# Kernel tuning notes

Measured on AMD Instinct MI355X. Metric: run time of the kernel, lower is better.

Reference implementation:

```python
import math
import jax, jax.numpy as jnp
import numpy as np

B, A, U, S, E, HYP, H = 16384, 32, 64, 2048, 32, 64, 4
ATTEND_REG_COEF = 1e-3


def setup_inputs() -> dict:
    key = jax.random.key(0)
    ks = jax.random.split(key, 12)
    sc = 0.05
    return {
        "agent_qs": jax.random.normal(ks[0], (B, A), jnp.float32),
        "states": jax.random.normal(ks[1], (B, S), jnp.float32),
        # per-head selector hypernet: Linear(S,HYP)+ReLU+Linear(HYP,E,no bias)
        "sel_w1": jax.random.normal(ks[2], (H, S, HYP), jnp.float32) * sc,
        "sel_b1": jax.random.normal(ks[3], (H, HYP), jnp.float32) * sc,
        "sel_w2": jax.random.normal(ks[4], (H, HYP, E), jnp.float32) * sc,
        # per-head key extractor: Linear(U,E,no bias)
        "key_w": jax.random.normal(ks[5], (H, U, E), jnp.float32) * sc,
        # V net: Linear(S,E)+ReLU+Linear(E,1)
        "v_w1": jax.random.normal(ks[6], (S, E), jnp.float32) * sc,
        "v_b1": jax.random.normal(ks[7], (E,), jnp.float32) * sc,
        "v_w2": jax.random.normal(ks[8], (E, 1), jnp.float32) * sc,
        "v_b2": jax.random.normal(ks[9], (1,), jnp.float32) * sc,
    }


def reference(agent_qs, states, sel_w1, sel_b1, sel_w2, key_w, v_w1, v_b1, v_w2, v_b2):
    # nonlinear=False, weighted_head=False, state_bias=True (defaults used here)
    unit_states = states[:, : A * U].reshape(-1, A, U)  # [B, A, U]

    # per-head selectors: [B, H, E]
    h1 = jax.nn.relu(jnp.einsum("bs,hsk->bhk", states, sel_w1) + sel_b1[None])
    selectors = jnp.einsum("bhk,hke->bhe", h1, sel_w2)

    # per-head, per-agent keys: [B, H, A, E]
    keys = jnp.einsum("bau,hue->bhae", unit_states, key_w)

    # attention logits [B, H, A] (matches selector @ stacked-keys in torch)
    logits = jnp.einsum("bhe,bhae->bha", selectors, keys)
    weights = jax.nn.softmax(logits / math.sqrt(E), axis=-1)  # [B, H, A]

    head_attend = jnp.sum(weights, axis=1)  # [B, A]

    v = jax.nn.relu(states @ v_w1 + v_b1) @ v_w2 + v_b2  # [B, 1]

    # coef * sum over heads of mean(logits_h ** 2)
    attend_mag_regs = ATTEND_REG_COEF * jnp.sum(jnp.mean(logits ** 2, axis=(0, 2)))

    # per-head entropy: -(p * log(p + 1e-8)).sum(agents).mean(batch) -> [H]
    head_entropies = -jnp.mean(
        jnp.sum(weights * jnp.log(weights + 1e-8), axis=-1), axis=0
    )

    return head_attend, v, attend_mag_regs, head_entropies
```

## Files before the change

kernel.cpp:

```cpp
#include <hip/hip_runtime.h>
#include <hip/hip_bf16.h>

#define B_N 16384
#define A_N 32
#define U_N 64
#define S_N 2048
#define E_N 32
#define HYP_N 64
#define H_N 4
#define NREAL 288
#define NPADG 320

#define H1B_STRIDE 264

#define WS_WT    0
#define WS_MB    1310720
#define WS_PMAG  (WS_MB + 32768)
#define WS_PENT  (WS_PMAG + 65536)
#define WS_T     (WS_PENT + 262144)
#define WS_HV    (WS_T + 16777216)

#define OUT_V   (B_N * A_N)
#define OUT_MAG (OUT_V + B_N)
#define OUT_ENT (OUT_MAG + 1)

typedef __attribute__((ext_vector_type(8))) short bf16x8_t;
typedef __attribute__((ext_vector_type(4))) float floatx4_t;

#define AS1(p) ((const __attribute__((address_space(1))) void*)(p))
#define AS3(p) ((__attribute__((address_space(3))) void*)(p))

__device__ __forceinline__ unsigned short f2b(float f) {
    union { float f; unsigned u; } v; v.f = f;
    unsigned r = v.u + 0x7FFFu + ((v.u >> 16) & 1u);
    return (unsigned short)(r >> 16);
}
__device__ __forceinline__ float b2f(unsigned x) {
    union { unsigned u; float f; } v; v.u = x << 16; return v.f;
}
__device__ __forceinline__ uint4 pack_bf16x8(float4 a0, float4 a1) {
    uint4 o;
    o.x = (unsigned)f2b(a0.x) | ((unsigned)f2b(a0.y) << 16);
    o.y = (unsigned)f2b(a0.z) | ((unsigned)f2b(a0.w) << 16);
    o.z = (unsigned)f2b(a1.x) | ((unsigned)f2b(a1.y) << 16);
    o.w = (unsigned)f2b(a1.z) | ((unsigned)f2b(a1.w) << 16);
    return o;
}

__global__ __launch_bounds__(256) void pack_w_kernel(
        const float* __restrict__ sel_w1, const float* __restrict__ v_w1,
        const float* __restrict__ sel_w2, const float* __restrict__ key_w,
        unsigned short* __restrict__ Wt, unsigned short* __restrict__ Mb) {
    int idx = blockIdx.x * 256 + threadIdx.x;
    if (idx < NPADG * S_N) {
        int n = idx >> 11;
        int k = idx & 2047;
        float val = 0.0f;
        if (n < 256) {
            int h = n >> 6, kk = n & 63;
            val = sel_w1[((size_t)h * S_N + k) * HYP_N + kk];
        } else if (n < NREAL) {
            val = v_w1[(size_t)k * E_N + (n - 256)];
        }
        Wt[idx] = f2b(val);
    } else if (idx < NPADG * S_N + H_N * U_N * HYP_N) {
        int j = idx - NPADG * S_N;
        int h = j >> 12, u = (j >> 6) & 63, k = j & 63;
        const float* kw = key_w + ((size_t)h * U_N + u) * E_N;
        const float* w2 = sel_w2 + ((size_t)h * HYP_N + k) * E_N;
        float s = 0.0f;
#pragma unroll
        for (int e = 0; e < E_N; ++e) s = fmaf(kw[e], w2[e], s);
        Mb[j] = f2b(s);
    }
}

#define FM_BM 64
#define FM_BK 64
#define NIT   (S_N / FM_BK)
#define ASM_SH (FM_BM * FM_BK)
#define BSM_SH (NPADG * FM_BK)

__global__ __launch_bounds__(512, 2) void gemm_t_kernel(
        const float* __restrict__ states, const unsigned short* __restrict__ Wt,
        const float* __restrict__ sel_b1, const float* __restrict__ v_b1,
        const unsigned short* __restrict__ Mb,
        float* __restrict__ tg, unsigned short* __restrict__ hv) {
    __shared__ __align__(16) char pool[2 * ASM_SH * 2 + 2 * BSM_SH * 2];
    unsigned short* Asm = (unsigned short*)pool;
    unsigned short* Bsm = (unsigned short*)(pool + 2 * ASM_SH * 2);
    unsigned short* h1b = (unsigned short*)pool;

    const int t = threadIdx.x;
    const int lane = t & 63;
    const int w = t >> 6;
    const int m0 = blockIdx.x * FM_BM;
    const int miw = (w & 1) * 32;
    const int nw = (w >> 1) * 80;

    const int ar = t >> 3, acl = t & 7;
    const float* ap = states + (size_t)(m0 + ar) * S_N + acl * 8;
    const int aph = acl ^ (ar & 7);

    floatx4_t acc[2][5] = {};
    float4 a0, a1;

    a0 = *(const float4*)(ap);
    a1 = *(const float4*)(ap + 4);
    *(uint4*)(Asm + (size_t)(ar * 8 + aph) * 8) = pack_bf16x8(a0, a1);
#pragma unroll
    for (int i = 0; i < 5; ++i) {
        int p = i * 512 + t, n = p >> 3, sl = p & 7;
        int cl = sl ^ (n & 7);
        __builtin_amdgcn_global_load_lds(AS1(Wt + (size_t)n * S_N + cl * 8),
                                         AS3(Bsm + p * 8), 16, 0, 0);
    }
    a0 = *(const float4*)(ap + FM_BK);
    a1 = *(const float4*)(ap + FM_BK + 4);
    __syncthreads();

    int cur = 0;
    for (int it = 0; it < NIT; ++it) {
        if (it < NIT - 1) {
            unsigned short* An = Asm + (cur ^ 1) * ASM_SH;
            unsigned short* Bn = Bsm + (cur ^ 1) * BSM_SH;
            int k0 = (it + 1) * FM_BK;
            *(uint4*)(An + (size_t)(ar * 8 + aph) * 8) = pack_bf16x8(a0, a1);
#pragma unroll
            for (int i = 0; i < 5; ++i) {
                int p = i * 512 + t, n = p >> 3, sl = p & 7;
                int cl = sl ^ (n & 7);
                __builtin_amdgcn_global_load_lds(
                    AS1(Wt + (size_t)n * S_N + k0 + cl * 8),
                    AS3(Bn + p * 8), 16, 0, 0);
            }
            if (it < NIT - 2) {
                const float* g = ap + (it + 2) * FM_BK;
                a0 = *(const float4*)(g);
                a1 = *(const float4*)(g + 4);
            }
        }
        const unsigned short* Ac = Asm + cur * ASM_SH;
        const unsigned short* Bc = Bsm + cur * BSM_SH;
#pragma unroll
        for (int s = 0; s < 2; ++s) {
            const int c = s * 4 + (lane >> 4);
            bf16x8_t afr[2];
#pragma unroll
            for (int mt = 0; mt < 2; ++mt) {
                int r = miw + mt * 16 + (lane & 15);
                afr[mt] = *(const bf16x8_t*)(Ac + r * 64 + (c ^ (r & 7)) * 8);
            }
#pragma unroll
            for (int nt = 0; nt < 5; ++nt) {
                int n = nw + nt * 16 + (lane & 15);
                bf16x8_t bfr = *(const bf16x8_t*)(Bc + n * 64 + (c ^ (n & 7)) * 8);
                acc[0][nt] = __builtin_amdgcn_mfma_f32_16x16x32_bf16(
                    afr[0], bfr, acc[0][nt], 0, 0, 0);
                acc[1][nt] = __builtin_amdgcn_mfma_f32_16x16x32_bf16(
                    afr[1], bfr, acc[1][nt], 0, 0, 0);
            }
        }
        __syncthreads();
        cur ^= 1;
    }

#pragma unroll
    for (int nt = 0; nt < 5; ++nt) {
        int n = nw + nt * 16 + (lane & 15);
        if (n < 256) {
            float bias = sel_b1[n];
#pragma unroll
            for (int mt = 0; mt < 2; ++mt)
#pragma unroll
                for (int rg = 0; rg < 4; ++rg) {
                    int r = miw + mt * 16 + (lane >> 4) * 4 + rg;
                    float v = acc[mt][nt][rg] + bias;
                    h1b[r * H1B_STRIDE + n] = f2b(v > 0.0f ? v : 0.0f);
                }
        } else if (n < NREAL) {
            int j = n - 256;
            float bias = v_b1[j];
#pragma unroll
            for (int mt = 0; mt < 2; ++mt)
#pragma unroll
                for (int rg = 0; rg < 4; ++rg) {
                    int r = miw + mt * 16 + (lane >> 4) * 4 + rg;
                    float v = acc[mt][nt][rg] + bias;
                    hv[(size_t)(m0 + r) * 32 + j] = f2b(v > 0.0f ? v : 0.0f);
                }
        }
    }
    __syncthreads();

    {
        const int h = w >> 1;
        const int rb = (w & 1) * 32;
        floatx4_t tacc[2][4] = {};
#pragma unroll
        for (int s = 0; s < 2; ++s) {
            int k0 = s * 32 + (lane >> 4) * 8;
            bf16x8_t afr[2];
#pragma unroll
            for (int mt = 0; mt < 2; ++mt)
                afr[mt] = *(const bf16x8_t*)(
                    h1b + (rb + mt * 16 + (lane & 15)) * H1B_STRIDE + h * 64 + k0);
#pragma unroll
            for (int ut = 0; ut < 4; ++ut) {
                int u = ut * 16 + (lane & 15);
                bf16x8_t bfr = *(const bf16x8_t*)(Mb + ((size_t)(h * U_N + u) * 64) + k0);
#pragma unroll
                for (int mt = 0; mt < 2; ++mt)
                    tacc[mt][ut] = __builtin_amdgcn_mfma_f32_16x16x32_bf16(
                        afr[mt], bfr, tacc[mt][ut], 0, 0, 0);
            }
        }
#pragma unroll
        for (int mt = 0; mt < 2; ++mt)
#pragma unroll
            for (int ut = 0; ut < 4; ++ut)
#pragma unroll
                for (int rg = 0; rg < 4; ++rg) {
                    int b = m0 + rb + mt * 16 + (lane >> 4) * 4 + rg;
                    int u = ut * 16 + (lane & 15);
                    tg[((size_t)b * H_N + h) * U_N + u] = tacc[mt][ut][rg];
                }
    }
}

#define L_BM 16

__global__ __launch_bounds__(256, 8) void attend_l_kernel(
        const float* __restrict__ states, const float* __restrict__ tg,
        const unsigned short* __restrict__ hv,
        const float* __restrict__ v_w2, const float* __restrict__ v_b2,
        float* __restrict__ out, float* __restrict__ pmag, float* __restrict__ pent) {
    const int t = threadIdx.x;
    const int lane = t & 63;
    const int w = t >> 6;
    const int m0 = blockIdx.x * L_BM;
    const int a = lane & 31, uh = lane >> 5;

    for (int rr = 0; rr < 4; ++rr) {
        const int b = m0 + w * 4 + rr;
        const float* up = states + (size_t)b * S_N + a * 64 + uh * 32;
        const float* tp = tg + (size_t)b * (H_N * U_N) + uh * 32;
        float pl[4] = {0.0f, 0.0f, 0.0f, 0.0f};
        float4 c0 = ((const float4*)up)[0];
        float4 c1 = ((const float4*)up)[1];
#pragma unroll
        for (int i = 0; i < 8; ++i) {
            float4 s4 = c0;
            c0 = c1;
            if (i < 6) c1 = ((const float4*)up)[i + 2];
#pragma unroll
            for (int h = 0; h < 4; ++h) {
                float4 t4 = *(const float4*)(tp + h * U_N + i * 4);
                pl[h] = fmaf(s4.x, t4.x, pl[h]);
                pl[h] = fmaf(s4.y, t4.y, pl[h]);
                pl[h] = fmaf(s4.z, t4.z, pl[h]);
                pl[h] = fmaf(s4.w, t4.w, pl[h]);
            }
        }
#pragma unroll
        for (int h = 0; h < 4; ++h)
            pl[h] += __shfl_xor(pl[h], 32, 64);

        float mg = pl[0]*pl[0] + pl[1]*pl[1] + pl[2]*pl[2] + pl[3]*pl[3];
#pragma unroll
        for (int o = 16; o > 0; o >>= 1) mg += __shfl_xor(mg, o, 32);

        float hatt = 0.0f;
        float entv[4];
#pragma unroll
        for (int h = 0; h < 4; ++h) {
            float x = pl[h] * 0.17677669529663687f;
            float p = __expf(x);
            float den = p, px = p * x;
#pragma unroll
            for (int o = 16; o > 0; o >>= 1) {
                den += __shfl_xor(den, o, 32);
                px  += __shfl_xor(px,  o, 32);
            }
            float inv = 1.0f / den;
            hatt = fmaf(p, inv, hatt);
            entv[h] = px * inv - __logf(den);
        }

        if (uh == 0) {
            out[(size_t)b * A_N + a] = hatt;
            float pv = b2f((unsigned)hv[(size_t)b * 32 + a]) * v_w2[a];
#pragma unroll
            for (int o = 16; o > 0; o >>= 1) pv += __shfl_xor(pv, o, 32);
            if (a == 0) {
                out[OUT_V + b] = pv + v_b2[0];
                pmag[b] = mg;
#pragma unroll
                for (int h = 0; h < 4; ++h) pent[(size_t)h * B_N + b] = entv[h];
            }
        }
    }
}

__global__ __launch_bounds__(256) void finalize_kernel(
        const float* __restrict__ pmag, const float* __restrict__ pent,
        float* __restrict__ out) {
    int which = blockIdx.x;
    const float* src = (which == 0) ? pmag : (pent + (size_t)(which - 1) * B_N);
    float s = 0.0f;
    for (int i = threadIdx.x; i < B_N; i += 256) s += src[i];
#pragma unroll
    for (int o = 32; o > 0; o >>= 1) s += __shfl_xor(s, o, 64);
    __shared__ float red[4];
    if ((threadIdx.x & 63) == 0) red[threadIdx.x >> 6] = s;
    __syncthreads();
    if (threadIdx.x == 0) {
        float tot = red[0] + red[1] + red[2] + red[3];
        if (which == 0) out[OUT_MAG] = 1e-3f * tot / (float)(B_N * A_N);
        else out[OUT_ENT + which - 1] = -tot / (float)B_N;
    }
}

extern "C" void kernel_launch(void* const* d_in, const int* in_sizes, int n_in,
                              void* d_out, int out_size, void* d_ws, size_t ws_size,
                              hipStream_t stream) {
    const float* states = (const float*)d_in[1];
    const float* sel_w1 = (const float*)d_in[2];
    const float* sel_b1 = (const float*)d_in[3];
    const float* sel_w2 = (const float*)d_in[4];
    const float* key_w  = (const float*)d_in[5];
    const float* v_w1   = (const float*)d_in[6];
    const float* v_b1   = (const float*)d_in[7];
    const float* v_w2   = (const float*)d_in[8];
    const float* v_b2   = (const float*)d_in[9];
    float* out = (float*)d_out;
    char* wsb  = (char*)d_ws;

    unsigned short* Wt  = (unsigned short*)(wsb + WS_WT);
    unsigned short* Mb  = (unsigned short*)(wsb + WS_MB);
    float* pmag         = (float*)(wsb + WS_PMAG);
    float* pent         = (float*)(wsb + WS_PENT);
    float* tg           = (float*)(wsb + WS_T);
    unsigned short* hv  = (unsigned short*)(wsb + WS_HV);

    pack_w_kernel<<<dim3((NPADG * S_N + H_N * U_N * HYP_N + 255) / 256),
                    dim3(256), 0, stream>>>(sel_w1, v_w1, sel_w2, key_w, Wt, Mb);
    gemm_t_kernel<<<dim3(B_N / FM_BM), dim3(512), 0, stream>>>(
        states, Wt, sel_b1, v_b1, Mb, tg, hv);
    attend_l_kernel<<<dim3(B_N / L_BM), dim3(256), 0, stream>>>(
        states, tg, hv, v_w2, v_b2, out, pmag, pent);
    finalize_kernel<<<dim3(5), dim3(256), 0, stream>>>(pmag, pent, out);
}
```

Baseline: 301.5 us.

## Halve GEMM row tile and drop LDS double buffering for higher occupancy

The fused states×weights GEMM kernel now uses 32-row tiles with 256 threads (4 waves, each covering 80 output columns) instead of 64 rows with 512 threads. The A and B shared-memory tiles lose their double buffering, which cuts LDS per block to about 45 KB so several blocks can be resident per CU and the grid doubles. The cost is that each block reloads the full 320-column weight tile for half as many rows, doubling weight traffic. Single buffering also adds a second barrier per K step, so loads no longer overlap with the MFMA work inside a block.

```diff
diff --git a/kernel.cpp b/kernel.cpp
--- a/kernel.cpp
+++ b/kernel.cpp
@@ -75,28 +75,25 @@
     }
 }
 
-#define FM_BM 64
+#define FM_BM 32
 #define FM_BK 64
 #define NIT   (S_N / FM_BK)
-#define ASM_SH (FM_BM * FM_BK)
-#define BSM_SH (NPADG * FM_BK)
-
-__global__ __launch_bounds__(512, 2) void gemm_t_kernel(
+
+__global__ __launch_bounds__(256, 3) void gemm_t_kernel(
         const float* __restrict__ states, const unsigned short* __restrict__ Wt,
         const float* __restrict__ sel_b1, const float* __restrict__ v_b1,
         const unsigned short* __restrict__ Mb,
         float* __restrict__ tg, unsigned short* __restrict__ hv) {
-    __shared__ __align__(16) char pool[2 * ASM_SH * 2 + 2 * BSM_SH * 2];
+    __shared__ __align__(16) char pool[4096 + 40960];
     unsigned short* Asm = (unsigned short*)pool;
-    unsigned short* Bsm = (unsigned short*)(pool + 2 * ASM_SH * 2);
+    unsigned short* Bsm = (unsigned short*)(pool + 4096);
     unsigned short* h1b = (unsigned short*)pool;
 
     const int t = threadIdx.x;
     const int lane = t & 63;
     const int w = t >> 6;
     const int m0 = blockIdx.x * FM_BM;
-    const int miw = (w & 1) * 32;
-    const int nw = (w >> 1) * 80;
+    const int nw = w * 80;
 
     const int ar = t >> 3, acl = t & 7;
     const float* ap = states + (size_t)(m0 + ar) * S_N + acl * 8;
@@ -109,8 +106,8 @@
     a1 = *(const float4*)(ap + 4);
     *(uint4*)(Asm + (size_t)(ar * 8 + aph) * 8) = pack_bf16x8(a0, a1);
 #pragma unroll
-    for (int i = 0; i < 5; ++i) {
-        int p = i * 512 + t, n = p >> 3, sl = p & 7;
+    for (int i = 0; i < 10; ++i) {
+        int p = i * 256 + t, n = p >> 3, sl = p & 7;
         int cl = sl ^ (n & 7);
         __builtin_amdgcn_global_load_lds(AS1(Wt + (size_t)n * S_N + cl * 8),
                                          AS3(Bsm + p * 8), 16, 0, 0);
@@ -119,50 +116,45 @@
     a1 = *(const float4*)(ap + FM_BK + 4);
     __syncthreads();
 
-    int cur = 0;
     for (int it = 0; it < NIT; ++it) {
+#pragma unroll
+        for (int s = 0; s < 2; ++s) {
+            const int c = s * 4 + (lane >> 4);
+            bf16x8_t afr[2];
+#pragma unroll
+            for (int mt = 0; mt < 2; ++mt) {
+                int r = mt * 16 + (lane & 15);
+                afr[mt] = *(const bf16x8_t*)(Asm + r * 64 + (c ^ (r & 7)) * 8);
+            }
+#pragma unroll
+            for (int nt = 0; nt < 5; ++nt) {
+                int n = nw + nt * 16 + (lane & 15);
+                bf16x8_t bfr = *(const bf16x8_t*)(Bsm + n * 64 + (c ^ (n & 7)) * 8);
+                acc[0][nt] = __builtin_amdgcn_mfma_f32_16x16x32_bf16(
+                    afr[0], bfr, acc[0][nt], 0, 0, 0);
+                acc[1][nt] = __builtin_amdgcn_mfma_f32_16x16x32_bf16(
+                    afr[1], bfr, acc[1][nt], 0, 0, 0);
+            }
+        }
+        __syncthreads();
         if (it < NIT - 1) {
-            unsigned short* An = Asm + (cur ^ 1) * ASM_SH;
-            unsigned short* Bn = Bsm + (cur ^ 1) * BSM_SH;
             int k0 = (it + 1) * FM_BK;
-            *(uint4*)(An + (size_t)(ar * 8 + aph) * 8) = pack_bf16x8(a0, a1);
-#pragma unroll
-            for (int i = 0; i < 5; ++i) {
-                int p = i * 512 + t, n = p >> 3, sl = p & 7;
+            *(uint4*)(Asm + (size_t)(ar * 8 + aph) * 8) = pack_bf16x8(a0, a1);
+#pragma unroll
+            for (int i = 0; i < 10; ++i) {
+                int p = i * 256 + t, n = p >> 3, sl = p & 7;
                 int cl = sl ^ (n & 7);
                 __builtin_amdgcn_global_load_lds(
                     AS1(Wt + (size_t)n * S_N + k0 + cl * 8),
-                    AS3(Bn + p * 8), 16, 0, 0);
+                    AS3(Bsm + p * 8), 16, 0, 0);
             }
             if (it < NIT - 2) {
                 const float* g = ap + (it + 2) * FM_BK;
                 a0 = *(const float4*)(g);
                 a1 = *(const float4*)(g + 4);
             }
-        }
-        const unsigned short* Ac = Asm + cur * ASM_SH;
-        const unsigned short* Bc = Bsm + cur * BSM_SH;
-#pragma unroll
-        for (int s = 0; s < 2; ++s) {
-            const int c = s * 4 + (lane >> 4);
-            bf16x8_t afr[2];
-#pragma unroll
-            for (int mt = 0; mt < 2; ++mt) {
-                int r = miw + mt * 16 + (lane & 15);
-                afr[mt] = *(const bf16x8_t*)(Ac + r * 64 + (c ^ (r & 7)) * 8);
-            }
-#pragma unroll
-            for (int nt = 0; nt < 5; ++nt) {
-                int n = nw + nt * 16 + (lane & 15);
-                bf16x8_t bfr = *(const bf16x8_t*)(Bc + n * 64 + (c ^ (n & 7)) * 8);
-                acc[0][nt] = __builtin_amdgcn_mfma_f32_16x16x32_bf16(
-                    afr[0], bfr, acc[0][nt], 0, 0, 0);
-                acc[1][nt] = __builtin_amdgcn_mfma_f32_16x16x32_bf16(
-                    afr[1], bfr, acc[1][nt], 0, 0, 0);
-            }
-        }
-        __syncthreads();
-        cur ^= 1;
+            __syncthreads();
+        }
     }
 
 #pragma unroll
@@ -174,7 +166,7 @@
             for (int mt = 0; mt < 2; ++mt)
 #pragma unroll
                 for (int rg = 0; rg < 4; ++rg) {
-                    int r = miw + mt * 16 + (lane >> 4) * 4 + rg;
+                    int r = mt * 16 + (lane >> 4) * 4 + rg;
                     float v = acc[mt][nt][rg] + bias;
                     h1b[r * H1B_STRIDE + n] = f2b(v > 0.0f ? v : 0.0f);
                 }
@@ -185,7 +177,7 @@
             for (int mt = 0; mt < 2; ++mt)
 #pragma unroll
                 for (int rg = 0; rg < 4; ++rg) {
-                    int r = miw + mt * 16 + (lane >> 4) * 4 + rg;
+                    int r = mt * 16 + (lane >> 4) * 4 + rg;
                     float v = acc[mt][nt][rg] + bias;
                     hv[(size_t)(m0 + r) * 32 + j] = f2b(v > 0.0f ? v : 0.0f);
                 }
@@ -194,8 +186,7 @@
     __syncthreads();
 
     {
-        const int h = w >> 1;
-        const int rb = (w & 1) * 32;
+        const int h = w;
         floatx4_t tacc[2][4] = {};
 #pragma unroll
         for (int s = 0; s < 2; ++s) {
@@ -204,7 +195,7 @@
 #pragma unroll
             for (int mt = 0; mt < 2; ++mt)
                 afr[mt] = *(const bf16x8_t*)(
-                    h1b + (rb + mt * 16 + (lane & 15)) * H1B_STRIDE + h * 64 + k0);
+                    h1b + (mt * 16 + (lane & 15)) * H1B_STRIDE + h * 64 + k0);
 #pragma unroll
             for (int ut = 0; ut < 4; ++ut) {
                 int u = ut * 16 + (lane & 15);
@@ -221,7 +212,7 @@
             for (int ut = 0; ut < 4; ++ut)
 #pragma unroll
                 for (int rg = 0; rg < 4; ++rg) {
-                    int b = m0 + rb + mt * 16 + (lane >> 4) * 4 + rg;
+                    int b = m0 + mt * 16 + (lane >> 4) * 4 + rg;
                     int u = ut * 16 + (lane & 15);
                     tg[((size_t)b * H_N + h) * U_N + u] = tacc[mt][ut][rg];
                 }
@@ -345,7 +336,7 @@
 
     pack_w_kernel<<<dim3((NPADG * S_N + H_N * U_N * HYP_N + 255) / 256),
                     dim3(256), 0, stream>>>(sel_w1, v_w1, sel_w2, key_w, Wt, Mb);
-    gemm_t_kernel<<<dim3(B_N / FM_BM), dim3(512), 0, stream>>>(
+    gemm_t_kernel<<<dim3(B_N / FM_BM), dim3(256), 0, stream>>>(
         states, Wt, sel_b1, v_b1, Mb, tg, hv);
     attend_l_kernel<<<dim3(B_N / L_BM), dim3(256), 0, stream>>>(
         states, tg, hv, v_w2, v_b2, out, pmag, pent);
```

After: 306.2 us. No clear change (+1.6%).

## Restructure GEMM mainloop with BK=32, deeper prefetch and raw barriers for occupancy

Applied to the files above, without the earlier changes.

Halves the K-tile to 32 so LDS per block shrinks and launch bounds allow four blocks per CU instead of two. The main loop is manually unrolled two steps at a time with explicit s_barrier and vmcnt waits, and A registers are prefetched four tiles ahead. The B tile is padded to 384 rows so 512 threads load it evenly with a new XOR swizzle. This is meant to overlap global loads with MFMA work and hide latency, at the cost of more barriers per unit of K and tighter register budgets.

```diff
diff --git a/kernel.cpp b/kernel.cpp
--- a/kernel.cpp
+++ b/kernel.cpp
@@ -10,11 +10,12 @@
 #define H_N 4
 #define NREAL 288
 #define NPADG 320
+#define NPS   384
 
 #define H1B_STRIDE 264
 
 #define WS_WT    0
-#define WS_MB    1310720
+#define WS_MB    1572864
 #define WS_PMAG  (WS_MB + 32768)
 #define WS_PENT  (WS_PMAG + 65536)
 #define WS_T     (WS_PENT + 262144)
@@ -38,12 +39,10 @@
 __device__ __forceinline__ float b2f(unsigned x) {
     union { unsigned u; float f; } v; v.u = x << 16; return v.f;
 }
-__device__ __forceinline__ uint4 pack_bf16x8(float4 a0, float4 a1) {
-    uint4 o;
-    o.x = (unsigned)f2b(a0.x) | ((unsigned)f2b(a0.y) << 16);
-    o.y = (unsigned)f2b(a0.z) | ((unsigned)f2b(a0.w) << 16);
-    o.z = (unsigned)f2b(a1.x) | ((unsigned)f2b(a1.y) << 16);
-    o.w = (unsigned)f2b(a1.z) | ((unsigned)f2b(a1.w) << 16);
+__device__ __forceinline__ uint2 pack_bf16x4(float4 a) {
+    uint2 o;
+    o.x = (unsigned)f2b(a.x) | ((unsigned)f2b(a.y) << 16);
+    o.y = (unsigned)f2b(a.z) | ((unsigned)f2b(a.w) << 16);
     return o;
 }
 
@@ -52,7 +51,7 @@
         const float* __restrict__ sel_w2, const float* __restrict__ key_w,
         unsigned short* __restrict__ Wt, unsigned short* __restrict__ Mb) {
     int idx = blockIdx.x * 256 + threadIdx.x;
-    if (idx < NPADG * S_N) {
+    if (idx < NPS * S_N) {
         int n = idx >> 11;
         int k = idx & 2047;
         float val = 0.0f;
@@ -63,8 +62,8 @@
             val = v_w1[(size_t)k * E_N + (n - 256)];
         }
         Wt[idx] = f2b(val);
-    } else if (idx < NPADG * S_N + H_N * U_N * HYP_N) {
-        int j = idx - NPADG * S_N;
+    } else if (idx < NPS * S_N + H_N * U_N * HYP_N) {
+        int j = idx - NPS * S_N;
         int h = j >> 12, u = (j >> 6) & 63, k = j & 63;
         const float* kw = key_w + ((size_t)h * U_N + u) * E_N;
         const float* w2 = sel_w2 + ((size_t)h * HYP_N + k) * E_N;
@@ -76,19 +75,62 @@
 }
 
 #define FM_BM 64
-#define FM_BK 64
+#define FM_BK 32
 #define NIT   (S_N / FM_BK)
-#define ASM_SH (FM_BM * FM_BK)
-#define BSM_SH (NPADG * FM_BK)
-
-__global__ __launch_bounds__(512, 2) void gemm_t_kernel(
+#define A_STRIDE 40
+#define ABUF_SH (FM_BM * A_STRIDE)
+#define BBUF_SH (NPS * FM_BK)
+
+#define GBODY(TT, AW)                                                          \
+    {                                                                          \
+        const int tt = (TT);                                                   \
+        const unsigned short* Ac = Asm + (tt & 1) * ABUF_SH;                   \
+        const unsigned short* Bc = Bsm + (tt & 1) * BBUF_SH;                   \
+        bf16x8_t af0 = *(const bf16x8_t*)(Ac + (miw + r) * A_STRIDE + q * 8);  \
+        bf16x8_t af1 = *(const bf16x8_t*)(Ac + (miw + 16 + r) * A_STRIDE + q * 8);\
+        _Pragma("unroll")                                                      \
+        for (int nt = 0; nt < 5; ++nt) {                                       \
+            int n = nw + nt * 16 + r;                                          \
+            bf16x8_t bfr = *(const bf16x8_t*)(                                 \
+                Bc + ((size_t)(n * 4 + (q ^ ((n >> 1) & 3))) * 8));            \
+            acc[0][nt] = __builtin_amdgcn_mfma_f32_16x16x32_bf16(              \
+                af0, bfr, acc[0][nt], 0, 0, 0);                                \
+            acc[1][nt] = __builtin_amdgcn_mfma_f32_16x16x32_bf16(              \
+                af1, bfr, acc[1][nt], 0, 0, 0);                                \
+        }                                                                      \
+        asm volatile("" ::: "memory");                                         \
+        __builtin_amdgcn_s_barrier();              \
+        asm volatile("" ::: "memory");                                         \
+        {                                                                      \
+            int ts = (tt + 2 < NIT) ? (tt + 2) : (NIT - 1);                    \
+            int k0 = ts * FM_BK;                                               \
+            unsigned short* Bn = Bsm + (tt & 1) * BBUF_SH;                     \
+            _Pragma("unroll")                                                  \
+            for (int i = 0; i < 3; ++i) {                                      \
+                int p = i * 512 + t;                                           \
+                int n = p >> 2;                                                \
+                int gl = (p & 3) ^ ((n >> 1) & 3);                             \
+                __builtin_amdgcn_global_load_lds(                              \
+                    AS1(Wt + (size_t)n * S_N + k0 + gl * 8),                   \
+                    AS3(Bn + (size_t)p * 8), 16, 0, 0);                        \
+            }                                                                  \
+            *(uint2*)(Asm + (tt & 1) * ABUF_SH + aoff) = pack_bf16x4(AW);      \
+            int la = (tt + 4 < NIT) ? (tt + 4) : (NIT - 1);                    \
+            AW = *(const float4*)(ap + la * FM_BK);                            \
+        }                                                                      \
+        asm volatile("s_waitcnt vmcnt(4) lgkmcnt(0)" ::: "memory");            \
+        __builtin_amdgcn_s_barrier();            \
+        asm volatile("" ::: "memory");                                         \
+    }
+
+__global__ __launch_bounds__(512, 4) void gemm_t_kernel(
         const float* __restrict__ states, const unsigned short* __restrict__ Wt,
         const float* __restrict__ sel_b1, const float* __restrict__ v_b1,
         const unsigned short* __restrict__ Mb,
         float* __restrict__ tg, unsigned short* __restrict__ hv) {
-    __shared__ __align__(16) char pool[2 * ASM_SH * 2 + 2 * BSM_SH * 2];
+    __shared__ __align__(16) char pool[2 * ABUF_SH * 2 + 2 * BBUF_SH * 2];
     unsigned short* Asm = (unsigned short*)pool;
-    unsigned short* Bsm = (unsigned short*)(pool + 2 * ASM_SH * 2);
+    unsigned short* Bsm = (unsigned short*)(pool + 2 * ABUF_SH * 2);
     unsigned short* h1b = (unsigned short*)pool;
 
     const int t = threadIdx.x;
@@ -97,73 +139,47 @@
     const int m0 = blockIdx.x * FM_BM;
     const int miw = (w & 1) * 32;
     const int nw = (w >> 1) * 80;
+    const int q = lane >> 4, r = lane & 15;
 
     const int ar = t >> 3, acl = t & 7;
-    const float* ap = states + (size_t)(m0 + ar) * S_N + acl * 8;
-    const int aph = acl ^ (ar & 7);
+    const float* ap = states + (size_t)(m0 + ar) * S_N + acl * 4;
+    const int aoff = ar * A_STRIDE + acl * 4;
 
     floatx4_t acc[2][5] = {};
-    float4 a0, a1;
-
-    a0 = *(const float4*)(ap);
-    a1 = *(const float4*)(ap + 4);
-    *(uint4*)(Asm + (size_t)(ar * 8 + aph) * 8) = pack_bf16x8(a0, a1);
-#pragma unroll
-    for (int i = 0; i < 5; ++i) {
-        int p = i * 512 + t, n = p >> 3, sl = p & 7;
-        int cl = sl ^ (n & 7);
-        __builtin_amdgcn_global_load_lds(AS1(Wt + (size_t)n * S_N + cl * 8),
-                                         AS3(Bsm + p * 8), 16, 0, 0);
-    }
-    a0 = *(const float4*)(ap + FM_BK);
-    a1 = *(const float4*)(ap + FM_BK + 4);
-    __syncthreads();
-
-    int cur = 0;
-    for (int it = 0; it < NIT; ++it) {
-        if (it < NIT - 1) {
-            unsigned short* An = Asm + (cur ^ 1) * ASM_SH;
-            unsigned short* Bn = Bsm + (cur ^ 1) * BSM_SH;
-            int k0 = (it + 1) * FM_BK;
-            *(uint4*)(An + (size_t)(ar * 8 + aph) * 8) = pack_bf16x8(a0, a1);
-#pragma unroll
-            for (int i = 0; i < 5; ++i) {
-                int p = i * 512 + t, n = p >> 3, sl = p & 7;
-                int cl = sl ^ (n & 7);
-                __builtin_amdgcn_global_load_lds(
-                    AS1(Wt + (size_t)n * S_N + k0 + cl * 8),
-                    AS3(Bn + p * 8), 16, 0, 0);
-            }
-            if (it < NIT - 2) {
-                const float* g = ap + (it + 2) * FM_BK;
-                a0 = *(const float4*)(g);
-                a1 = *(const float4*)(g + 4);
-            }
-        }
-        const unsigned short* Ac = Asm + cur * ASM_SH;
-        const unsigned short* Bc = Bsm + cur * BSM_SH;
-#pragma unroll
-        for (int s = 0; s < 2; ++s) {
-            const int c = s * 4 + (lane >> 4);
-            bf16x8_t afr[2];
-#pragma unroll
-            for (int mt = 0; mt < 2; ++mt) {
-                int r = miw + mt * 16 + (lane & 15);
-                afr[mt] = *(const bf16x8_t*)(Ac + r * 64 + (c ^ (r & 7)) * 8);
-            }
-#pragma unroll
-            for (int nt = 0; nt < 5; ++nt) {
-                int n = nw + nt * 16 + (lane & 15);
-                bf16x8_t bfr = *(const bf16x8_t*)(Bc + n * 64 + (c ^ (n & 7)) * 8);
-                acc[0][nt] = __builtin_amdgcn_mfma_f32_16x16x32_bf16(
-                    afr[0], bfr, acc[0][nt], 0, 0, 0);
-                acc[1][nt] = __builtin_amdgcn_mfma_f32_16x16x32_bf16(
-                    afr[1], bfr, acc[1][nt], 0, 0, 0);
-            }
-        }
-        __syncthreads();
-        cur ^= 1;
-    }
+    float4 aX, aY;
+
+    aX = *(const float4*)(ap);
+#pragma unroll
+    for (int i = 0; i < 3; ++i) {
+        int p = i * 512 + t, n = p >> 2;
+        int gl = (p & 3) ^ ((n >> 1) & 3);
+        __builtin_amdgcn_global_load_lds(AS1(Wt + (size_t)n * S_N + gl * 8),
+                                         AS3(Bsm + (size_t)p * 8), 16, 0, 0);
+    }
+    *(uint2*)(Asm + aoff) = pack_bf16x4(aX);
+    aX = *(const float4*)(ap + FM_BK);
+#pragma unroll
+    for (int i = 0; i < 3; ++i) {
+        int p = i * 512 + t, n = p >> 2;
+        int gl = (p & 3) ^ ((n >> 1) & 3);
+        __builtin_amdgcn_global_load_lds(AS1(Wt + (size_t)n * S_N + FM_BK + gl * 8),
+                                         AS3(Bsm + BBUF_SH + (size_t)p * 8), 16, 0, 0);
+    }
+    *(uint2*)(Asm + ABUF_SH + aoff) = pack_bf16x4(aX);
+    aX = *(const float4*)(ap + 2 * FM_BK);
+    aY = *(const float4*)(ap + 3 * FM_BK);
+    asm volatile("s_waitcnt lgkmcnt(0)" ::: "memory");
+    __builtin_amdgcn_s_barrier();
+    asm volatile("" ::: "memory");
+
+    for (int it2 = 0; it2 < NIT / 2; ++it2) {
+        GBODY(it2 * 2,     aX);
+        GBODY(it2 * 2 + 1, aY);
+    }
+
+    asm volatile("s_waitcnt vmcnt(0) lgkmcnt(0)" ::: "memory");
+    __builtin_amdgcn_s_barrier();
+    asm volatile("" ::: "memory");
 
 #pragma unroll
     for (int nt = 0; nt < 5; ++nt) {
@@ -174,9 +190,9 @@
             for (int mt = 0; mt < 2; ++mt)
 #pragma unroll
                 for (int rg = 0; rg < 4; ++rg) {
-                    int r = miw + mt * 16 + (lane >> 4) * 4 + rg;
+                    int rr = miw + mt * 16 + (lane >> 4) * 4 + rg;
                     float v = acc[mt][nt][rg] + bias;
-                    h1b[r * H1B_STRIDE + n] = f2b(v > 0.0f ? v : 0.0f);
+                    h1b[rr * H1B_STRIDE + n] = f2b(v > 0.0f ? v : 0.0f);
                 }
         } else if (n < NREAL) {
             int j = n - 256;
@@ -185,9 +201,9 @@
             for (int mt = 0; mt < 2; ++mt)
 #pragma unroll
                 for (int rg = 0; rg < 4; ++rg) {
-                    int r = miw + mt * 16 + (lane >> 4) * 4 + rg;
+                    int rr = miw + mt * 16 + (lane >> 4) * 4 + rg;
                     float v = acc[mt][nt][rg] + bias;
-                    hv[(size_t)(m0 + r) * 32 + j] = f2b(v > 0.0f ? v : 0.0f);
+                    hv[(size_t)(m0 + rr) * 32 + j] = f2b(v > 0.0f ? v : 0.0f);
                 }
         }
     }
@@ -343,7 +359,7 @@
     float* tg           = (float*)(wsb + WS_T);
     unsigned short* hv  = (unsigned short*)(wsb + WS_HV);
 
-    pack_w_kernel<<<dim3((NPADG * S_N + H_N * U_N * HYP_N + 255) / 256),
+    pack_w_kernel<<<dim3((NPS * S_N + H_N * U_N * HYP_N + 255) / 256),
                     dim3(256), 0, stream>>>(sel_w1, v_w1, sel_w2, key_w, Wt, Mb);
     gemm_t_kernel<<<dim3(B_N / FM_BM), dim3(512), 0, stream>>>(
         states, Wt, sel_b1, v_b1, Mb, tg, hv);
```

Measured after the change: 314.9 us. 4.5% more time.
